# Kernel optimization log

Measured on AMD Instinct MI355X. Metric: run time of the kernel, lower is better.

The kernel has to match this reference:

```python
import jax, jax.numpy as jnp
import numpy as np

EMBED = 768
HEAD = 64

def setup_inputs() -> dict:
    key = jax.random.key(0)
    k1, k2, k3, k4 = jax.random.split(key, 4)
    x = jax.random.normal(k1, (8, 2048, EMBED), dtype=jnp.float32)
    # torch nn.Linear weights: [out, in], applied as x @ W.T
    scale = 1.0 / np.sqrt(EMBED)
    Wq = jax.random.uniform(k2, (HEAD, EMBED), jnp.float32, -scale, scale)
    Wk = jax.random.uniform(k3, (HEAD, EMBED), jnp.float32, -scale, scale)
    Wv = jax.random.uniform(k4, (HEAD, EMBED), jnp.float32, -scale, scale)
    return {"x": x, "Wq": Wq, "Wk": Wk, "Wv": Wv}

def reference(x, Wq, Wk, Wv):
    B, S, E = x.shape
    q = jnp.einsum('bse,he->bsh', x, Wq)
    k = jnp.einsum('bse,he->bsh', x, Wk)
    v = jnp.einsum('bse,he->bsh', x, Wv)
    # NOTE: faithful to source: weights / embed**(-0.5) == weights * sqrt(embed)
    scores = jnp.einsum('bqh,bkh->bqk', q, k) * jnp.sqrt(jnp.float32(E))
    causal = jnp.tril(jnp.ones((S, S), dtype=bool))
    scores = jnp.where(causal, scores, -jnp.inf)
    attn = jax.nn.softmax(scores, axis=-1)
    return jnp.einsum('bqk,bkh->bqh', attn, v)
```

## Files before the change

### kernel.cpp

```cpp
#include <hip/hip_runtime.h>
#include <math.h>

#define EMBED 768
#define SEQ   2048
#define NB    8
#define QSCALE 39.98113776623437f

typedef short  short4v __attribute__((ext_vector_type(4)));
typedef short  short8 __attribute__((ext_vector_type(8)));
typedef float  f32x4  __attribute__((ext_vector_type(4)));
typedef float  f32x16 __attribute__((ext_vector_type(16)));
typedef unsigned int uint2v __attribute__((ext_vector_type(2)));

#define WHI_OFF  0u
#define WLO_OFF  147456u
#define QHI_OFF  294912u
#define QLO_OFF  (294912u + 1u*1048576u)
#define KHI_OFF  (294912u + 2u*1048576u)
#define KLO_OFF  (294912u + 3u*1048576u)
#define VT_OFF   (294912u + 4u*1048576u)
#define OPU_OFF  5537792u
#define MPL_OFF  (5537792u + 8u*1048576u)

__device__ __forceinline__ ushort f2bf(float f) {
    unsigned u = __float_as_uint(f);
    return (ushort)((u + 0x7FFFu + ((u >> 16) & 1u)) >> 16);
}
__device__ __forceinline__ ushort f2bf_trunc(float f) {
    return (ushort)(__float_as_uint(f) >> 16);
}
__device__ __forceinline__ float bf2f(ushort h) {
    return __uint_as_float(((unsigned)h) << 16);
}
__device__ __forceinline__ uint cvtpk(float a, float b) {
    uint r;
    asm("v_cvt_pk_bf16_f32 %0, %1, %2" : "=v"(r) : "v"(a), "v"(b));
    return r;
}

union U8 { uint u[4]; short8 s; };

__global__ __launch_bounds__(256)
void split_w_kernel(const float* __restrict__ Wq, const float* __restrict__ Wk,
                    const float* __restrict__ Wv,
                    ushort* __restrict__ w_hi, ushort* __restrict__ w_lo)
{
    int idx = blockIdx.x * 256 + threadIdx.x;
    if (idx >= 192 * EMBED) return;
    int row = idx / EMBED, e = idx - row * EMBED;
    float f;
    if (row < 64)       f = Wq[row * EMBED + e] * QSCALE;
    else if (row < 128) f = Wk[(row - 64) * EMBED + e];
    else                f = Wv[(row - 128) * EMBED + e];
    ushort hi = f2bf(f);
    w_hi[idx] = hi;
    w_lo[idx] = f2bf_trunc(f - bf2f(hi));
}

__global__ __launch_bounds__(512)
void proj_kernel(const float* __restrict__ x,
                 const ushort* __restrict__ w_hi, const ushort* __restrict__ w_lo,
                 ushort* __restrict__ q_hi, ushort* __restrict__ q_lo,
                 ushort* __restrict__ k_hi, ushort* __restrict__ k_lo,
                 ushort* __restrict__ v_t)
{
    __shared__ __align__(16) ushort xah[2][64][72], xal[2][64][72];
    __shared__ __align__(16) ushort wbh[2][192][72];
    __shared__ __align__(16) ushort wbl[2][128][72];

    const int t    = threadIdx.x;
    const int lane = t & 63;
    const int wid  = t >> 6;
    const int wm   = wid >> 2;
    const int wn   = wid & 3;
    const int ln   = lane & 15;
    const int kg   = lane >> 4;
    const int row0 = blockIdx.x * 64;

#define LOADSET(e0, XR0, XR1, WH0, WH1, WH2, WL0, WL1) do {                       \
        const float* xp_ = x + (size_t)(row0 + (t >> 4)) * EMBED + (e0) + (t & 15) * 4; \
        XR0 = *(const float4*)xp_;                                                \
        XR1 = *(const float4*)(xp_ + 32 * EMBED);                                 \
        const ushort* wp_ = w_hi + (size_t)(t >> 3) * EMBED + (e0) + (t & 7) * 8; \
        WH0 = *(const short8*)wp_;                                                \
        WH1 = *(const short8*)(wp_ + 64 * EMBED);                                 \
        WH2 = *(const short8*)(wp_ + 128 * EMBED);                                \
        const ushort* lp_ = w_lo + (size_t)(t >> 3) * EMBED + (e0) + (t & 7) * 8; \
        WL0 = *(const short8*)lp_;                                                \
        WL1 = *(const short8*)(lp_ + 64 * EMBED);                                 \
    } while (0)

#define STORESET(BUF, XR0, XR1, WH0, WH1, WH2, WL0, WL1) do {                     \
        const int xr_ = t >> 4, xc_ = (t & 15) * 4;                               \
        const float f0_[4] = {XR0.x, XR0.y, XR0.z, XR0.w};                        \
        const float f1_[4] = {XR1.x, XR1.y, XR1.z, XR1.w};                        \
        short4v h0_, l0_, h1_, l1_;                                               \
        _Pragma("unroll")                                                         \
        for (int i_ = 0; i_ < 4; ++i_) {                                          \
            ushort h_ = f2bf(f0_[i_]);                                            \
            h0_[i_] = (short)h_;                                                  \
            l0_[i_] = (short)f2bf_trunc(f0_[i_] - bf2f(h_));                      \
        }                                                                         \
        _Pragma("unroll")                                                         \
        for (int i_ = 0; i_ < 4; ++i_) {                                          \
            ushort h_ = f2bf(f1_[i_]);                                            \
            h1_[i_] = (short)h_;                                                  \
            l1_[i_] = (short)f2bf_trunc(f1_[i_] - bf2f(h_));                      \
        }                                                                         \
        *(short4v*)&xah[BUF][xr_][xc_]      = h0_;                                \
        *(short4v*)&xal[BUF][xr_][xc_]      = l0_;                                \
        *(short4v*)&xah[BUF][xr_ + 32][xc_] = h1_;                                \
        *(short4v*)&xal[BUF][xr_ + 32][xc_] = l1_;                                \
        const int wr_ = t >> 3, wc_ = (t & 7) * 8;                                \
        *(short8*)&wbh[BUF][wr_][wc_]       = WH0;                                \
        *(short8*)&wbh[BUF][wr_ + 64][wc_]  = WH1;                                \
        *(short8*)&wbh[BUF][wr_ + 128][wc_] = WH2;                                \
        *(short8*)&wbl[BUF][wr_][wc_]       = WL0;                                \
        *(short8*)&wbl[BUF][wr_ + 64][wc_]  = WL1;                                \
    } while (0)

#define COMPUTE(BUF) do {                                                         \
        short8 ah_[2][2], al_[2][2];                                              \
        _Pragma("unroll")                                                         \
        for (int mt_ = 0; mt_ < 2; ++mt_)                                         \
            _Pragma("unroll")                                                     \
            for (int ks_ = 0; ks_ < 2; ++ks_) {                                   \
                ah_[mt_][ks_] = *(const short8*)&xah[BUF][wm * 32 + mt_ * 16 + ln][ks_ * 32 + kg * 8]; \
                al_[mt_][ks_] = *(const short8*)&xal[BUF][wm * 32 + mt_ * 16 + ln][ks_ * 32 + kg * 8]; \
            }                                                                     \
        _Pragma("unroll")                                                         \
        for (int j_ = 0; j_ < 3; ++j_) {                                          \
            const int ntg_ = j_ * 4 + wn;                                         \
            _Pragma("unroll")                                                     \
            for (int ks_ = 0; ks_ < 2; ++ks_) {                                   \
                const int co_ = ks_ * 32 + kg * 8;                                \
                short8 bh_ = *(const short8*)&wbh[BUF][ntg_ * 16 + ln][co_];      \
                _Pragma("unroll")                                                 \
                for (int mt_ = 0; mt_ < 2; ++mt_)                                 \
                    acc[mt_][j_] = __builtin_amdgcn_mfma_f32_16x16x32_bf16(ah_[mt_][ks_], bh_, acc[mt_][j_], 0, 0, 0); \
                if (j_ < 2) {                                                     \
                    short8 bl_ = *(const short8*)&wbl[BUF][ntg_ * 16 + ln][co_];  \
                    _Pragma("unroll")                                             \
                    for (int mt_ = 0; mt_ < 2; ++mt_) {                           \
                        acc[mt_][j_] = __builtin_amdgcn_mfma_f32_16x16x32_bf16(ah_[mt_][ks_], bl_, acc[mt_][j_], 0, 0, 0); \
                        acc[mt_][j_] = __builtin_amdgcn_mfma_f32_16x16x32_bf16(al_[mt_][ks_], bh_, acc[mt_][j_], 0, 0, 0); \
                    }                                                             \
                }                                                                 \
            }                                                                     \
        }                                                                         \
    } while (0)

    const f32x4 vzero = {0.f, 0.f, 0.f, 0.f};
    f32x4 acc[2][3];
#pragma unroll
    for (int mt = 0; mt < 2; ++mt)
#pragma unroll
        for (int j = 0; j < 3; ++j) acc[mt][j] = vzero;

    float4 xrA0, xrA1; short8 whA0, whA1, whA2, wlA0, wlA1;
    float4 xrB0, xrB1; short8 whB0, whB1, whB2, wlB0, wlB1;
    float4 xrC0, xrC1; short8 whC0, whC1, whC2, wlC0, wlC1;

    LOADSET(0,   xrA0, xrA1, whA0, whA1, whA2, wlA0, wlA1);
    LOADSET(64,  xrB0, xrB1, whB0, whB1, whB2, wlB0, wlB1);
    LOADSET(128, xrC0, xrC1, whC0, whC1, whC2, wlC0, wlC1);

#define ITER(C_, VMC, BUF, X0, X1, W0, W1, W2, L0, L1) do {                       \
        asm volatile("s_waitcnt vmcnt(" #VMC ")" ::: "memory");                   \
        STORESET(BUF, X0, X1, W0, W1, W2, L0, L1);                                \
        asm volatile("s_waitcnt lgkmcnt(0)" ::: "memory");                        \
        __builtin_amdgcn_s_barrier();                                             \
        if ((C_) + 3 < 12) LOADSET(((C_) + 3) * 64, X0, X1, W0, W1, W2, L0, L1);  \
        COMPUTE(BUF);                                                             \
    } while (0)

    ITER(0,  14, 0, xrA0, xrA1, whA0, whA1, whA2, wlA0, wlA1);
    ITER(1,  14, 1, xrB0, xrB1, whB0, whB1, whB2, wlB0, wlB1);
    ITER(2,  14, 0, xrC0, xrC1, whC0, whC1, whC2, wlC0, wlC1);
    ITER(3,  14, 1, xrA0, xrA1, whA0, whA1, whA2, wlA0, wlA1);
    ITER(4,  14, 0, xrB0, xrB1, whB0, whB1, whB2, wlB0, wlB1);
    ITER(5,  14, 1, xrC0, xrC1, whC0, whC1, whC2, wlC0, wlC1);
    ITER(6,  14, 0, xrA0, xrA1, whA0, whA1, whA2, wlA0, wlA1);
    ITER(7,  14, 1, xrB0, xrB1, whB0, whB1, whB2, wlB0, wlB1);
    ITER(8,  14, 0, xrC0, xrC1, whC0, whC1, whC2, wlC0, wlC1);
    ITER(9,  14, 1, xrA0, xrA1, whA0, whA1, whA2, wlA0, wlA1);
    ITER(10,  7, 0, xrB0, xrB1, whB0, whB1, whB2, wlB0, wlB1);
    ITER(11,  0, 1, xrC0, xrC1, whC0, whC1, whC2, wlC0, wlC1);
#undef ITER
#undef LOADSET
#undef STORESET
#undef COMPUTE

#pragma unroll
    for (int mt = 0; mt < 2; ++mt) {
        const int rbase = row0 + wm * 32 + mt * 16 + kg * 4;
#pragma unroll
        for (int j = 0; j < 3; ++j) {
            const int col = (j * 4 + wn) * 16 + ln;
#pragma unroll
            for (int r = 0; r < 4; ++r) {
                int rg = rbase + r;
                int b = rg >> 11, s = rg & 2047;
                size_t rowoff = ((size_t)b * SEQ + s) * 64;
                float val = acc[mt][j][r];
                if (col < 64) {
                    ushort h = f2bf(val);
                    q_hi[rowoff + col] = h;
                    q_lo[rowoff + col] = f2bf_trunc(val - bf2f(h));
                } else if (col < 128) {
                    ushort h = f2bf(val);
                    k_hi[rowoff + (col - 64)] = h;
                    k_lo[rowoff + (col - 64)] = f2bf_trunc(val - bf2f(h));
                } else {
                    v_t[((size_t)b * 64 + (col - 128)) * SEQ + s] = f2bf(val);
                }
            }
        }
    }
}

__global__ __launch_bounds__(256)
void attn_kernel(const ushort* __restrict__ q_hi, const ushort* __restrict__ q_lo,
                 const ushort* __restrict__ k_hi, const ushort* __restrict__ k_lo,
                 const ushort* __restrict__ v_t,
                 ushort* __restrict__ oP, float* __restrict__ mP,
                 float* __restrict__ lP, int Z)
{
    __shared__ __align__(16) ushort kv[3][3][64][64];

    const int t    = threadIdx.x;
    const int lane = t & 63;
    const int w    = t >> 6;
    const int l31  = lane & 31;
    const int h8   = (lane >> 5) << 3;
    const int sw   = (lane & 7) << 3;
    const int b    = blockIdx.x & 7;
    const int pr   = (blockIdx.x >> 3) & 7;
    const int z    = blockIdx.x >> 6;
    const int qA   = 15 - pr;
    const int qB   = pr;
    const int cA   = 2 * qA + 2;
    const int T    = 34;

    const ushort* qhb = q_hi + (size_t)b * SEQ * 64;
    const ushort* qlb = q_lo + (size_t)b * SEQ * 64;
    const ushort* khb = k_hi + (size_t)b * SEQ * 64;
    const ushort* klb = k_lo + (size_t)b * SEQ * 64;
    const ushort* vtb = v_t + (size_t)b * 64 * SEQ;
    ushort* oPz = oP + (size_t)z * 1048576u;
    float*  mPz = mP + (size_t)z * 16384u;
    float*  lPz = lP + (size_t)z * 16384u;

    const int srow8 = lane >> 3;
    const int scol  = ((lane & 7) << 3) ^ ((lane >> 3) << 3);

    auto stage = [&](int g, int cbuf) {
        const int kk = (g < cA) ? g : g - cA;
        const int j0 = kk << 6;
        ushort* base = &kv[cbuf][0][0][0];
#pragma unroll
        for (int s = 0; s < 6; ++s) {
            const int i = w * 6 + s;
            const int row = ((i & 7) << 3) + srow8;
            const ushort* gp;
            if (i < 8)       gp = khb + (size_t)(j0 + row) * 64 + scol;
            else if (i < 16) gp = klb + (size_t)(j0 + row) * 64 + scol;
            else             gp = vtb + (size_t)row * SEQ + j0 + scol;
            __builtin_amdgcn_global_load_lds(
                (const __attribute__((address_space(1))) void*)gp,
                (__attribute__((address_space(3))) void*)(base + i * 512),
                16, 0, 0);
        }
    };

    auto loadQ = [&](int qb, short8 (&qh)[4], short8 (&ql)[4]) {
#pragma unroll
        for (int ks = 0; ks < 4; ++ks) {
            size_t off = (size_t)(qb * 128 + w * 32 + l31) * 64 + ks * 16 + h8;
            qh[ks] = *(const short8*)(qhb + off);
            ql[ks] = *(const short8*)(qlb + off);
        }
// ... 142 lines not shown
        __builtin_amdgcn_s_barrier();
        if (i + 2 < cnt) stage(z + (i + 2) * Z, (i + 2) % 3);
        if (g >= cA && !inB) {
            storeP(qA, o, m_run, l_run);
            loadQ(qB, qh, ql);
#pragma unroll
            for (int j = 0; j < 16; ++j) { o[0][j] = 0.f; o[1][j] = 0.f; }
            m_run = -INFINITY; l_run = 0.f;
            inB = true;
        }
        body(g < cA ? g : g - cA, g < cA ? qA : qB, o, m_run, l_run, qh, ql, i % 3);
    }

    if (!inB) {
        storeP(qA, o, m_run, l_run);
        const size_t rowq = (size_t)b * SEQ + qB * 128 + w * 32 + l31;
        ushort* op = oPz + rowq * 64;
        const int hb = (lane >> 5) << 2;
#pragma unroll
        for (int ht = 0; ht < 2; ++ht)
#pragma unroll
            for (int rq = 0; rq < 4; ++rq) {
                *(uint*)(op + ht * 32 + rq * 8 + hb)     = 0u;
                *(uint*)(op + ht * 32 + rq * 8 + hb + 2) = 0u;
            }
        if (lane < 32) { mPz[rowq] = -INFINITY; lPz[rowq] = 0.f; }
    } else {
        storeP(qB, o, m_run, l_run);
    }
}

__global__ __launch_bounds__(256)
void merge_kernel(const ushort* __restrict__ oP, const float* __restrict__ mP,
                  const float* __restrict__ lP, float* __restrict__ out, int Z)
{
    int idx = blockIdx.x * 256 + threadIdx.x;
    int R  = idx >> 4;
    int h0 = (idx & 15) << 2;
    float M = -INFINITY;
    for (int zz = 0; zz < Z; ++zz) M = fmaxf(M, mP[zz * 16384 + R]);
    float L = 0.f;
    float4 acc = make_float4(0.f, 0.f, 0.f, 0.f);
    for (int zz = 0; zz < Z; ++zz) {
        float c = exp2f(mP[zz * 16384 + R] - M);
        L += lP[zz * 16384 + R] * c;
        const ushort* op = oP + (size_t)zz * 1048576u + (size_t)R * 64 + h0;
        uint u0 = *(const uint*)op;
        uint u1 = *(const uint*)(op + 2);
        acc.x += bf2f((ushort)(u0 & 0xFFFFu)) * c;
        acc.y += bf2f((ushort)(u0 >> 16))     * c;
        acc.z += bf2f((ushort)(u1 & 0xFFFFu)) * c;
        acc.w += bf2f((ushort)(u1 >> 16))     * c;
    }
    float inv = 1.0f / L;
    float4 r = make_float4(acc.x * inv, acc.y * inv, acc.z * inv, acc.w * inv);
    *(float4*)(out + (size_t)R * 64 + h0) = r;
}

extern "C" void kernel_launch(void* const* d_in, const int* in_sizes, int n_in,
                              void* d_out, int out_size, void* d_ws, size_t ws_size,
                              hipStream_t stream)
{
    const float* x  = (const float*)d_in[0];
    const float* Wq = (const float*)d_in[1];
    const float* Wk = (const float*)d_in[2];
    const float* Wv = (const float*)d_in[3];
    float* out = (float*)d_out;

    ushort* ws = (ushort*)d_ws;
    ushort* w_hi = ws + WHI_OFF;
    ushort* w_lo = ws + WLO_OFF;
    ushort* q_hi = ws + QHI_OFF;
    ushort* q_lo = ws + QLO_OFF;
    ushort* k_hi = ws + KHI_OFF;
    ushort* k_lo = ws + KLO_OFF;
    ushort* v_t  = ws + VT_OFF;

    const int Z = 8;
    ushort* oP = ws + OPU_OFF;
    float*  mP = (float*)(ws + MPL_OFF);
    float*  lP = mP + (size_t)Z * 16384u;

    split_w_kernel<<<dim3(576), dim3(256), 0, stream>>>(Wq, Wk, Wv, w_hi, w_lo);
    proj_kernel<<<dim3(256), dim3(512), 0, stream>>>(x, w_hi, w_lo,
                                                     q_hi, q_lo, k_hi, k_lo, v_t);
    attn_kernel<<<dim3(64 * Z), dim3(256), 0, stream>>>(q_hi, q_lo, k_hi, k_lo, v_t,
                                                        oP, mP, lP, Z);
    merge_kernel<<<dim3(1024), dim3(256), 0, stream>>>(oP, mP, lP, out, Z);
}
```

Baseline: 55.58 us.

## Load weights via direct global-to-LDS with swizzle; split x in registers

The projection kernel now copies the bf16 hi/lo weight tiles straight into LDS with global_load_lds into a triple-buffered, XOR-swizzled layout. x is no longer staged through shared memory: each lane loads its own MFMA fragment rows from global and splits them into bf16 hi/lo pairs in registers with packed converts. The pipeline changes to a two-stage prefetch, and MFMA sections run at raised priority. This removes the LDS stores and the lgkmcnt wait for x and the weights. In exchange, the per-lane x loads are less coalesced and use more registers.

After: 69.03 us. 24.2% more time.

```diff
diff --git a/kernel.cpp b/kernel.cpp
--- a/kernel.cpp
+++ b/kernel.cpp
@@ -6,7 +6,6 @@
 #define NB    8
 #define QSCALE 39.98113776623437f
 
-typedef short  short4v __attribute__((ext_vector_type(4)));
 typedef short  short8 __attribute__((ext_vector_type(8)));
 typedef float  f32x4  __attribute__((ext_vector_type(4)));
 typedef float  f32x16 __attribute__((ext_vector_type(16)));
@@ -36,6 +35,12 @@
     uint r;
     asm("v_cvt_pk_bf16_f32 %0, %1, %2" : "=v"(r) : "v"(a), "v"(b));
     return r;
+}
+__device__ __forceinline__ float pklo(uint h) {
+    return __uint_as_float(h << 16);
+}
+__device__ __forceinline__ float pkhi(uint h) {
+    return __uint_as_float(h & 0xFFFF0000u);
 }
 
 union U8 { uint u[4]; short8 s; };
@@ -64,9 +69,7 @@
                  ushort* __restrict__ k_hi, ushort* __restrict__ k_lo,
                  ushort* __restrict__ v_t)
 {
-    __shared__ __align__(16) ushort xah[2][64][72], xal[2][64][72];
-    __shared__ __align__(16) ushort wbh[2][192][72];
-    __shared__ __align__(16) ushort wbl[2][128][72];
+    __shared__ __align__(16) ushort wb[3][20480];
 
     const int t    = threadIdx.x;
     const int lane = t & 63;
@@ -77,118 +80,126 @@
     const int kg   = lane >> 4;
     const int row0 = blockIdx.x * 64;
 
-#define LOADSET(e0, XR0, XR1, WH0, WH1, WH2, WL0, WL1) do {                       \
-        const float* xp_ = x + (size_t)(row0 + (t >> 4)) * EMBED + (e0) + (t & 15) * 4; \
-        XR0 = *(const float4*)xp_;                                                \
-        XR1 = *(const float4*)(xp_ + 32 * EMBED);                                 \
-        const ushort* wp_ = w_hi + (size_t)(t >> 3) * EMBED + (e0) + (t & 7) * 8; \
-        WH0 = *(const short8*)wp_;                                                \
-        WH1 = *(const short8*)(wp_ + 64 * EMBED);                                 \
-        WH2 = *(const short8*)(wp_ + 128 * EMBED);                                \
-        const ushort* lp_ = w_lo + (size_t)(t >> 3) * EMBED + (e0) + (t & 7) * 8; \
-        WL0 = *(const short8*)lp_;                                                \
-        WL1 = *(const short8*)(lp_ + 64 * EMBED);                                 \
+    const int srow8 = lane >> 3;
+    const int scol  = ((lane & 7) << 3) ^ ((lane >> 3) << 3);
+
+    auto stageW = [&](int c, int bf) {
+        const int e0 = c * 64;
+        ushort* base = &wb[bf][0];
+#pragma unroll
+        for (int s = 0; s < 5; ++s) {
+            const int i = wid * 5 + s;
+            if (i < 24) {
+                const int row = i * 8 + srow8;
+                const ushort* gp = w_hi + (size_t)row * EMBED + e0 + scol;
+                __builtin_amdgcn_global_load_lds(
+                    (const __attribute__((address_space(1))) void*)gp,
+                    (__attribute__((address_space(3))) void*)(base + i * 512),
+                    16, 0, 0);
+            } else {
+                const int il = i - 24;
+                const int row = il * 8 + srow8;
+                const ushort* gp = w_lo + (size_t)row * EMBED + e0 + scol;
+                __builtin_amdgcn_global_load_lds(
+                    (const __attribute__((address_space(1))) void*)gp,
+                    (__attribute__((address_space(3))) void*)(base + 12288 + il * 512),
+                    16, 0, 0);
+            }
+        }
+    };
+
+#define XLOAD(e0, R) do {                                                        \
+        const float* xp_ = x + (size_t)(row0 + wm * 32 + ln) * EMBED + (e0) + kg * 8; \
+        R[0] = *(const float4*)xp_;                                              \
+        R[1] = *(const float4*)(xp_ + 4);                                        \
+        R[2] = *(const float4*)(xp_ + 32);                                       \
+        R[3] = *(const float4*)(xp_ + 36);                                       \
+        R[4] = *(const float4*)(xp_ + 16 * EMBED);                               \
+        R[5] = *(const float4*)(xp_ + 16 * EMBED + 4);                           \
+        R[6] = *(const float4*)(xp_ + 16 * EMBED + 32);                          \
+        R[7] = *(const float4*)(xp_ + 16 * EMBED + 36);                          \
     } while (0)
 
-#define STORESET(BUF, XR0, XR1, WH0, WH1, WH2, WL0, WL1) do {                     \
-        const int xr_ = t >> 4, xc_ = (t & 15) * 4;                               \
-        const float f0_[4] = {XR0.x, XR0.y, XR0.z, XR0.w};                        \
-        const float f1_[4] = {XR1.x, XR1.y, XR1.z, XR1.w};                        \
-        short4v h0_, l0_, h1_, l1_;                                               \
-        _Pragma("unroll")                                                         \
-        for (int i_ = 0; i_ < 4; ++i_) {                                          \
-            ushort h_ = f2bf(f0_[i_]);                                            \
-            h0_[i_] = (short)h_;                                                  \
-            l0_[i_] = (short)f2bf_trunc(f0_[i_] - bf2f(h_));                      \
-        }                                                                         \
-        _Pragma("unroll")                                                         \
-        for (int i_ = 0; i_ < 4; ++i_) {                                          \
-            ushort h_ = f2bf(f1_[i_]);                                            \
-            h1_[i_] = (short)h_;                                                  \
-            l1_[i_] = (short)f2bf_trunc(f1_[i_] - bf2f(h_));                      \
-        }                                                                         \
-        *(short4v*)&xah[BUF][xr_][xc_]      = h0_;                                \
-        *(short4v*)&xal[BUF][xr_][xc_]      = l0_;                                \
-        *(short4v*)&xah[BUF][xr_ + 32][xc_] = h1_;                                \
-        *(short4v*)&xal[BUF][xr_ + 32][xc_] = l1_;                                \
-        const int wr_ = t >> 3, wc_ = (t & 7) * 8;                                \
-        *(short8*)&wbh[BUF][wr_][wc_]       = WH0;                                \
-        *(short8*)&wbh[BUF][wr_ + 64][wc_]  = WH1;                                \
-        *(short8*)&wbh[BUF][wr_ + 128][wc_] = WH2;                                \
-        *(short8*)&wbl[BUF][wr_][wc_]       = WL0;                                \
-        *(short8*)&wbl[BUF][wr_ + 64][wc_]  = WL1;                                \
-    } while (0)
-
-#define COMPUTE(BUF) do {                                                         \
-        short8 ah_[2][2], al_[2][2];                                              \
+    const f32x4 vzero = {0.f, 0.f, 0.f, 0.f};
+    f32x4 acc[2][3];
+#pragma unroll
+    for (int mt = 0; mt < 2; ++mt)
+#pragma unroll
+        for (int j = 0; j < 3; ++j) acc[mt][j] = vzero;
+
+#define COMPUTE(BF, R) do {                                                       \
+        const ushort* WHB_ = &wb[BF][0];                                          \
+        const ushort* WLB_ = &wb[BF][12288];                                      \
+        U8 ah_[2][2], al_[2][2];                                                  \
         _Pragma("unroll")                                                         \
         for (int mt_ = 0; mt_ < 2; ++mt_)                                         \
             _Pragma("unroll")                                                     \
             for (int ks_ = 0; ks_ < 2; ++ks_) {                                   \
-                ah_[mt_][ks_] = *(const short8*)&xah[BUF][wm * 32 + mt_ * 16 + ln][ks_ * 32 + kg * 8]; \
-                al_[mt_][ks_] = *(const short8*)&xal[BUF][wm * 32 + mt_ * 16 + ln][ks_ * 32 + kg * 8]; \
+                float4 a_ = R[mt_ * 4 + ks_ * 2];                                 \
+                float4 b_ = R[mt_ * 4 + ks_ * 2 + 1];                             \
+                U8 H_, L_;                                                        \
+                H_.u[0] = cvtpk(a_.x, a_.y);  H_.u[1] = cvtpk(a_.z, a_.w);        \
+                H_.u[2] = cvtpk(b_.x, b_.y);  H_.u[3] = cvtpk(b_.z, b_.w);        \
+                L_.u[0] = cvtpk(a_.x - pklo(H_.u[0]), a_.y - pkhi(H_.u[0]));      \
+                L_.u[1] = cvtpk(a_.z - pklo(H_.u[1]), a_.w - pkhi(H_.u[1]));      \
+                L_.u[2] = cvtpk(b_.x - pklo(H_.u[2]), b_.y - pkhi(H_.u[2]));      \
+                L_.u[3] = cvtpk(b_.z - pklo(H_.u[3]), b_.w - pkhi(H_.u[3]));      \
+                ah_[mt_][ks_] = H_;  al_[mt_][ks_] = L_;                          \
             }                                                                     \
+        __builtin_amdgcn_s_setprio(1);                                            \
         _Pragma("unroll")                                                         \
         for (int j_ = 0; j_ < 3; ++j_) {                                          \
             const int ntg_ = j_ * 4 + wn;                                         \
             _Pragma("unroll")                                                     \
             for (int ks_ = 0; ks_ < 2; ++ks_) {                                   \
-                const int co_ = ks_ * 32 + kg * 8;                                \
-                short8 bh_ = *(const short8*)&wbh[BUF][ntg_ * 16 + ln][co_];      \
+                const int rw_  = ntg_ * 16 + ln;                                  \
+                const int off_ = rw_ * 64 + ((ks_ * 32 + kg * 8) ^ ((rw_ & 7) << 3)); \
+                short8 bh_ = *(const short8*)(WHB_ + off_);                       \
                 _Pragma("unroll")                                                 \
                 for (int mt_ = 0; mt_ < 2; ++mt_)                                 \
-                    acc[mt_][j_] = __builtin_amdgcn_mfma_f32_16x16x32_bf16(ah_[mt_][ks_], bh_, acc[mt_][j_], 0, 0, 0); \
+                    acc[mt_][j_] = __builtin_amdgcn_mfma_f32_16x16x32_bf16(ah_[mt_][ks_].s, bh_, acc[mt_][j_], 0, 0, 0); \
                 if (j_ < 2) {                                                     \
-                    short8 bl_ = *(const short8*)&wbl[BUF][ntg_ * 16 + ln][co_];  \
+                    short8 bl_ = *(const short8*)(WLB_ + off_);                   \
                     _Pragma("unroll")                                             \
                     for (int mt_ = 0; mt_ < 2; ++mt_) {                           \
-                        acc[mt_][j_] = __builtin_amdgcn_mfma_f32_16x16x32_bf16(ah_[mt_][ks_], bl_, acc[mt_][j_], 0, 0, 0); \
-                        acc[mt_][j_] = __builtin_amdgcn_mfma_f32_16x16x32_bf16(al_[mt_][ks_], bh_, acc[mt_][j_], 0, 0, 0); \
+                        acc[mt_][j_] = __builtin_amdgcn_mfma_f32_16x16x32_bf16(ah_[mt_][ks_].s, bl_, acc[mt_][j_], 0, 0, 0); \
+                        acc[mt_][j_] = __builtin_amdgcn_mfma_f32_16x16x32_bf16(al_[mt_][ks_].s, bh_, acc[mt_][j_], 0, 0, 0); \
                     }                                                             \
                 }                                                                 \
             }                                                                     \
         }                                                                         \
+        __builtin_amdgcn_s_setprio(0);                                            \
     } while (0)
 
-    const f32x4 vzero = {0.f, 0.f, 0.f, 0.f};
-    f32x4 acc[2][3];
-#pragma unroll
-    for (int mt = 0; mt < 2; ++mt)
-#pragma unroll
-        for (int j = 0; j < 3; ++j) acc[mt][j] = vzero;
-
-    float4 xrA0, xrA1; short8 whA0, whA1, whA2, wlA0, wlA1;
-    float4 xrB0, xrB1; short8 whB0, whB1, whB2, wlB0, wlB1;
-    float4 xrC0, xrC1; short8 whC0, whC1, whC2, wlC0, wlC1;
-
-    LOADSET(0,   xrA0, xrA1, whA0, whA1, whA2, wlA0, wlA1);
-    LOADSET(64,  xrB0, xrB1, whB0, whB1, whB2, wlB0, wlB1);
-    LOADSET(128, xrC0, xrC1, whC0, whC1, whC2, wlC0, wlC1);
-
-#define ITER(C_, VMC, BUF, X0, X1, W0, W1, W2, L0, L1) do {                       \
+    float4 xr0[8], xr1[8], xr2[8];
+
+    stageW(0, 0); XLOAD(0,  xr0);
+    stageW(1, 1); XLOAD(64, xr1);
+
+#define ITER(C_, VMC, RSET, RNEXT) do {                                           \
         asm volatile("s_waitcnt vmcnt(" #VMC ")" ::: "memory");                   \
-        STORESET(BUF, X0, X1, W0, W1, W2, L0, L1);                                \
-        asm volatile("s_waitcnt lgkmcnt(0)" ::: "memory");                        \
         __builtin_amdgcn_s_barrier();                                             \
-        if ((C_) + 3 < 12) LOADSET(((C_) + 3) * 64, X0, X1, W0, W1, W2, L0, L1);  \
-        COMPUTE(BUF);                                                             \
+        if ((C_) + 2 < 12) {                                                      \
+            stageW((C_) + 2, ((C_) + 2) % 3);                                     \
+            XLOAD(((C_) + 2) * 64, RNEXT);                                        \
+        }                                                                         \
+        COMPUTE((C_) % 3, RSET);                                                  \
     } while (0)
 
-    ITER(0,  14, 0, xrA0, xrA1, whA0, whA1, whA2, wlA0, wlA1);
-    ITER(1,  14, 1, xrB0, xrB1, whB0, whB1, whB2, wlB0, wlB1);
-    ITER(2,  14, 0, xrC0, xrC1, whC0, whC1, whC2, wlC0, wlC1);
-    ITER(3,  14, 1, xrA0, xrA1, whA0, whA1, whA2, wlA0, wlA1);
-    ITER(4,  14, 0, xrB0, xrB1, whB0, whB1, whB2, wlB0, wlB1);
-    ITER(5,  14, 1, xrC0, xrC1, whC0, whC1, whC2, wlC0, wlC1);
-    ITER(6,  14, 0, xrA0, xrA1, whA0, whA1, whA2, wlA0, wlA1);
-    ITER(7,  14, 1, xrB0, xrB1, whB0, whB1, whB2, wlB0, wlB1);
-    ITER(8,  14, 0, xrC0, xrC1, whC0, whC1, whC2, wlC0, wlC1);
-    ITER(9,  14, 1, xrA0, xrA1, whA0, whA1, whA2, wlA0, wlA1);
-    ITER(10,  7, 0, xrB0, xrB1, whB0, whB1, whB2, wlB0, wlB1);
-    ITER(11,  0, 1, xrC0, xrC1, whC0, whC1, whC2, wlC0, wlC1);
+    ITER(0,  13, xr0, xr2);
+    ITER(1,  13, xr1, xr0);
+    ITER(2,  13, xr2, xr1);
+    ITER(3,  13, xr0, xr2);
+    ITER(4,  13, xr1, xr0);
+    ITER(5,  13, xr2, xr1);
+    ITER(6,  13, xr0, xr2);
+    ITER(7,  13, xr1, xr0);
+    ITER(8,  13, xr2, xr1);
+    ITER(9,  13, xr0, xr2);
+    ITER(10, 13, xr1, xr0);
+    ITER(11,  0, xr2, xr0);
 #undef ITER
-#undef LOADSET
-#undef STORESET
+#undef XLOAD
 #undef COMPUTE
 
 #pragma unroll
```

## Shrink projection tiles to 32 rows and 32-wide K steps for more blocks

Applied to the files above, without the earlier changes.

The projection kernel now uses 256-thread blocks covering 32 rows each, with 32-wide K chunks over 24 pipelined iterations, so the grid grows from 256 to 512 blocks to better fill the GPU's compute units. It also raises wave priority around the MFMA section with s_setprio. The cost is that each block re-reads the full weight matrix for half as many rows, doubling weight traffic, and each K step does less work per barrier, so barrier overhead grows.

Result: slower. 66.80 us (+20.2%).

```diff
diff --git a/kernel.cpp b/kernel.cpp
--- a/kernel.cpp
+++ b/kernel.cpp
@@ -57,61 +57,49 @@
     w_lo[idx] = f2bf_trunc(f - bf2f(hi));
 }
 
-__global__ __launch_bounds__(512)
+__global__ __launch_bounds__(256)
 void proj_kernel(const float* __restrict__ x,
                  const ushort* __restrict__ w_hi, const ushort* __restrict__ w_lo,
                  ushort* __restrict__ q_hi, ushort* __restrict__ q_lo,
                  ushort* __restrict__ k_hi, ushort* __restrict__ k_lo,
                  ushort* __restrict__ v_t)
 {
-    __shared__ __align__(16) ushort xah[2][64][72], xal[2][64][72];
-    __shared__ __align__(16) ushort wbh[2][192][72];
-    __shared__ __align__(16) ushort wbl[2][128][72];
+    __shared__ __align__(16) ushort xah[2][32][40], xal[2][32][40];
+    __shared__ __align__(16) ushort wbh[2][192][40];
+    __shared__ __align__(16) ushort wbl[2][128][40];
 
     const int t    = threadIdx.x;
     const int lane = t & 63;
-    const int wid  = t >> 6;
-    const int wm   = wid >> 2;
-    const int wn   = wid & 3;
+    const int w    = t >> 6;
     const int ln   = lane & 15;
     const int kg   = lane >> 4;
-    const int row0 = blockIdx.x * 64;
-
-#define LOADSET(e0, XR0, XR1, WH0, WH1, WH2, WL0, WL1) do {                       \
-        const float* xp_ = x + (size_t)(row0 + (t >> 4)) * EMBED + (e0) + (t & 15) * 4; \
-        XR0 = *(const float4*)xp_;                                                \
-        XR1 = *(const float4*)(xp_ + 32 * EMBED);                                 \
-        const ushort* wp_ = w_hi + (size_t)(t >> 3) * EMBED + (e0) + (t & 7) * 8; \
+    const int row0 = blockIdx.x * 32;
+
+#define LOADSET(e0, XR, WH0, WH1, WH2, WL0, WL1) do {                             \
+        const float* xp_ = x + (size_t)(row0 + (t >> 3)) * EMBED + (e0) + (t & 7) * 4; \
+        XR = *(const float4*)xp_;                                                 \
+        const ushort* wp_ = w_hi + (size_t)(t >> 2) * EMBED + (e0) + (t & 3) * 8; \
         WH0 = *(const short8*)wp_;                                                \
         WH1 = *(const short8*)(wp_ + 64 * EMBED);                                 \
         WH2 = *(const short8*)(wp_ + 128 * EMBED);                                \
-        const ushort* lp_ = w_lo + (size_t)(t >> 3) * EMBED + (e0) + (t & 7) * 8; \
+        const ushort* lp_ = w_lo + (size_t)(t >> 2) * EMBED + (e0) + (t & 3) * 8; \
         WL0 = *(const short8*)lp_;                                                \
         WL1 = *(const short8*)(lp_ + 64 * EMBED);                                 \
     } while (0)
 
-#define STORESET(BUF, XR0, XR1, WH0, WH1, WH2, WL0, WL1) do {                     \
-        const int xr_ = t >> 4, xc_ = (t & 15) * 4;                               \
-        const float f0_[4] = {XR0.x, XR0.y, XR0.z, XR0.w};                        \
-        const float f1_[4] = {XR1.x, XR1.y, XR1.z, XR1.w};                        \
-        short4v h0_, l0_, h1_, l1_;                                               \
+#define STORESET(BUF, XR, WH0, WH1, WH2, WL0, WL1) do {                           \
+        const int xr_ = t >> 3, xc_ = (t & 7) * 4;                                \
+        const float fv_[4] = {XR.x, XR.y, XR.z, XR.w};                            \
+        short4v h_, l_;                                                           \
         _Pragma("unroll")                                                         \
         for (int i_ = 0; i_ < 4; ++i_) {                                          \
-            ushort h_ = f2bf(f0_[i_]);                                            \
-            h0_[i_] = (short)h_;                                                  \
-            l0_[i_] = (short)f2bf_trunc(f0_[i_] - bf2f(h_));                      \
+            ushort hh_ = f2bf(fv_[i_]);                                           \
+            h_[i_] = (short)hh_;                                                  \
+            l_[i_] = (short)f2bf_trunc(fv_[i_] - bf2f(hh_));                      \
         }                                                                         \
-        _Pragma("unroll")                                                         \
-        for (int i_ = 0; i_ < 4; ++i_) {                                          \
-            ushort h_ = f2bf(f1_[i_]);                                            \
-            h1_[i_] = (short)h_;                                                  \
-            l1_[i_] = (short)f2bf_trunc(f1_[i_] - bf2f(h_));                      \
-        }                                                                         \
-        *(short4v*)&xah[BUF][xr_][xc_]      = h0_;                                \
-        *(short4v*)&xal[BUF][xr_][xc_]      = l0_;                                \
-        *(short4v*)&xah[BUF][xr_ + 32][xc_] = h1_;                                \
-        *(short4v*)&xal[BUF][xr_ + 32][xc_] = l1_;                                \
-        const int wr_ = t >> 3, wc_ = (t & 7) * 8;                                \
+        *(short4v*)&xah[BUF][xr_][xc_] = h_;                                      \
+        *(short4v*)&xal[BUF][xr_][xc_] = l_;                                      \
+        const int wr_ = t >> 2, wc_ = (t & 3) * 8;                                \
         *(short8*)&wbh[BUF][wr_][wc_]       = WH0;                                \
         *(short8*)&wbh[BUF][wr_ + 64][wc_]  = WH1;                                \
         *(short8*)&wbh[BUF][wr_ + 128][wc_] = WH2;                                \
@@ -120,34 +108,30 @@
     } while (0)
 
 #define COMPUTE(BUF) do {                                                         \
-        short8 ah_[2][2], al_[2][2];                                              \
+        short8 ah_[2], al_[2];                                                    \
         _Pragma("unroll")                                                         \
-        for (int mt_ = 0; mt_ < 2; ++mt_)                                         \
-            _Pragma("unroll")                                                     \
-            for (int ks_ = 0; ks_ < 2; ++ks_) {                                   \
-                ah_[mt_][ks_] = *(const short8*)&xah[BUF][wm * 32 + mt_ * 16 + ln][ks_ * 32 + kg * 8]; \
-                al_[mt_][ks_] = *(const short8*)&xal[BUF][wm * 32 + mt_ * 16 + ln][ks_ * 32 + kg * 8]; \
-            }                                                                     \
+        for (int mt_ = 0; mt_ < 2; ++mt_) {                                       \
+            ah_[mt_] = *(const short8*)&xah[BUF][mt_ * 16 + ln][kg * 8];          \
+            al_[mt_] = *(const short8*)&xal[BUF][mt_ * 16 + ln][kg * 8];          \
+        }                                                                         \
+        __builtin_amdgcn_s_setprio(1);                                            \
         _Pragma("unroll")                                                         \
         for (int j_ = 0; j_ < 3; ++j_) {                                          \
-            const int ntg_ = j_ * 4 + wn;                                         \
+            const int ntg_ = j_ * 4 + w;                                          \
+            short8 bh_ = *(const short8*)&wbh[BUF][ntg_ * 16 + ln][kg * 8];       \
             _Pragma("unroll")                                                     \
-            for (int ks_ = 0; ks_ < 2; ++ks_) {                                   \
-                const int co_ = ks_ * 32 + kg * 8;                                \
-                short8 bh_ = *(const short8*)&wbh[BUF][ntg_ * 16 + ln][co_];      \
+            for (int mt_ = 0; mt_ < 2; ++mt_)                                     \
+                acc[mt_][j_] = __builtin_amdgcn_mfma_f32_16x16x32_bf16(ah_[mt_], bh_, acc[mt_][j_], 0, 0, 0); \
+            if (j_ < 2) {                                                         \
+                short8 bl_ = *(const short8*)&wbl[BUF][ntg_ * 16 + ln][kg * 8];   \
                 _Pragma("unroll")                                                 \
-                for (int mt_ = 0; mt_ < 2; ++mt_)                                 \
-                    acc[mt_][j_] = __builtin_amdgcn_mfma_f32_16x16x32_bf16(ah_[mt_][ks_], bh_, acc[mt_][j_], 0, 0, 0); \
-                if (j_ < 2) {                                                     \
-                    short8 bl_ = *(const short8*)&wbl[BUF][ntg_ * 16 + ln][co_];  \
-                    _Pragma("unroll")                                             \
-                    for (int mt_ = 0; mt_ < 2; ++mt_) {                           \
-                        acc[mt_][j_] = __builtin_amdgcn_mfma_f32_16x16x32_bf16(ah_[mt_][ks_], bl_, acc[mt_][j_], 0, 0, 0); \
-                        acc[mt_][j_] = __builtin_amdgcn_mfma_f32_16x16x32_bf16(al_[mt_][ks_], bh_, acc[mt_][j_], 0, 0, 0); \
-                    }                                                             \
+                for (int mt_ = 0; mt_ < 2; ++mt_) {                               \
+                    acc[mt_][j_] = __builtin_amdgcn_mfma_f32_16x16x32_bf16(ah_[mt_], bl_, acc[mt_][j_], 0, 0, 0); \
+                    acc[mt_][j_] = __builtin_amdgcn_mfma_f32_16x16x32_bf16(al_[mt_], bh_, acc[mt_][j_], 0, 0, 0); \
                 }                                                                 \
             }                                                                     \
         }                                                                         \
+        __builtin_amdgcn_s_setprio(0);                                            \
     } while (0)
 
     const f32x4 vzero = {0.f, 0.f, 0.f, 0.f};
@@ -157,35 +141,47 @@
 #pragma unroll
         for (int j = 0; j < 3; ++j) acc[mt][j] = vzero;
 
-    float4 xrA0, xrA1; short8 whA0, whA1, whA2, wlA0, wlA1;
-    float4 xrB0, xrB1; short8 whB0, whB1, whB2, wlB0, wlB1;
-    float4 xrC0, xrC1; short8 whC0, whC1, whC2, wlC0, wlC1;
-
-    LOADSET(0,   xrA0, xrA1, whA0, whA1, whA2, wlA0, wlA1);
-    LOADSET(64,  xrB0, xrB1, whB0, whB1, whB2, wlB0, wlB1);
-    LOADSET(128, xrC0, xrC1, whC0, whC1, whC2, wlC0, wlC1);
-
-#define ITER(C_, VMC, BUF, X0, X1, W0, W1, W2, L0, L1) do {                       \
+    float4 xA; short8 hA0, hA1, hA2, lA0, lA1;
+    float4 xB; short8 hB0, hB1, hB2, lB0, lB1;
+    float4 xC; short8 hC0, hC1, hC2, lC0, lC1;
+
+    LOADSET(0,  xA, hA0, hA1, hA2, lA0, lA1);
+    LOADSET(32, xB, hB0, hB1, hB2, lB0, lB1);
+    LOADSET(64, xC, hC0, hC1, hC2, lC0, lC1);
+
+#define ITER(C_, VMC, XR, W0, W1, W2, L0, L1) do {                                \
         asm volatile("s_waitcnt vmcnt(" #VMC ")" ::: "memory");                   \
-        STORESET(BUF, X0, X1, W0, W1, W2, L0, L1);                                \
+        STORESET((C_) & 1, XR, W0, W1, W2, L0, L1);                               \
         asm volatile("s_waitcnt lgkmcnt(0)" ::: "memory");                        \
         __builtin_amdgcn_s_barrier();                                             \
-        if ((C_) + 3 < 12) LOADSET(((C_) + 3) * 64, X0, X1, W0, W1, W2, L0, L1);  \
-        COMPUTE(BUF);                                                             \
+        if ((C_) + 3 < 24) LOADSET(((C_) + 3) * 32, XR, W0, W1, W2, L0, L1);      \
+        COMPUTE((C_) & 1);                                                        \
     } while (0)
 
-    ITER(0,  14, 0, xrA0, xrA1, whA0, whA1, whA2, wlA0, wlA1);
-    ITER(1,  14, 1, xrB0, xrB1, whB0, whB1, whB2, wlB0, wlB1);
-    ITER(2,  14, 0, xrC0, xrC1, whC0, whC1, whC2, wlC0, wlC1);
-    ITER(3,  14, 1, xrA0, xrA1, whA0, whA1, whA2, wlA0, wlA1);
-    ITER(4,  14, 0, xrB0, xrB1, whB0, whB1, whB2, wlB0, wlB1);
-    ITER(5,  14, 1, xrC0, xrC1, whC0, whC1, whC2, wlC0, wlC1);
-    ITER(6,  14, 0, xrA0, xrA1, whA0, whA1, whA2, wlA0, wlA1);
-    ITER(7,  14, 1, xrB0, xrB1, whB0, whB1, whB2, wlB0, wlB1);
-    ITER(8,  14, 0, xrC0, xrC1, whC0, whC1, whC2, wlC0, wlC1);
-    ITER(9,  14, 1, xrA0, xrA1, whA0, whA1, whA2, wlA0, wlA1);
-    ITER(10,  7, 0, xrB0, xrB1, whB0, whB1, whB2, wlB0, wlB1);
-    ITER(11,  0, 1, xrC0, xrC1, whC0, whC1, whC2, wlC0, wlC1);
+    ITER(0,  12, xA, hA0, hA1, hA2, lA0, lA1);
+    ITER(1,  12, xB, hB0, hB1, hB2, lB0, lB1);
+    ITER(2,  12, xC, hC0, hC1, hC2, lC0, lC1);
+    ITER(3,  12, xA, hA0, hA1, hA2, lA0, lA1);
+    ITER(4,  12, xB, hB0, hB1, hB2, lB0, lB1);
+    ITER(5,  12, xC, hC0, hC1, hC2, lC0, lC1);
+    ITER(6,  12, xA, hA0, hA1, hA2, lA0, lA1);
+    ITER(7,  12, xB, hB0, hB1, hB2, lB0, lB1);
+    ITER(8,  12, xC, hC0, hC1, hC2, lC0, lC1);
+    ITER(9,  12, xA, hA0, hA1, hA2, lA0, lA1);
+    ITER(10, 12, xB, hB0, hB1, hB2, lB0, lB1);
+    ITER(11, 12, xC, hC0, hC1, hC2, lC0, lC1);
+    ITER(12, 12, xA, hA0, hA1, hA2, lA0, lA1);
+    ITER(13, 12, xB, hB0, hB1, hB2, lB0, lB1);
+    ITER(14, 12, xC, hC0, hC1, hC2, lC0, lC1);
+    ITER(15, 12, xA, hA0, hA1, hA2, lA0, lA1);
+    ITER(16, 12, xB, hB0, hB1, hB2, lB0, lB1);
+    ITER(17, 12, xC, hC0, hC1, hC2, lC0, lC1);
+    ITER(18, 12, xA, hA0, hA1, hA2, lA0, lA1);
+    ITER(19, 12, xB, hB0, hB1, hB2, lB0, lB1);
+    ITER(20, 12, xC, hC0, hC1, hC2, lC0, lC1);
+    ITER(21, 12, xA, hA0, hA1, hA2, lA0, lA1);
+    ITER(22,  6, xB, hB0, hB1, hB2, lB0, lB1);
+    ITER(23,  0, xC, hC0, hC1, hC2, lC0, lC1);
 #undef ITER
 #undef LOADSET
 #undef STORESET
@@ -193,10 +189,10 @@
 
 #pragma unroll
     for (int mt = 0; mt < 2; ++mt) {
-        const int rbase = row0 + wm * 32 + mt * 16 + kg * 4;
+        const int rbase = row0 + mt * 16 + kg * 4;
 #pragma unroll
         for (int j = 0; j < 3; ++j) {
-            const int col = (j * 4 + wn) * 16 + ln;
+            const int col = (j * 4 + w) * 16 + ln;
 #pragma unroll
             for (int r = 0; r < 4; ++r) {
                 int rg = rbase + r;
@@ -505,7 +501,7 @@
     float*  lP = mP + (size_t)Z * 16384u;
 
     split_w_kernel<<<dim3(576), dim3(256), 0, stream>>>(Wq, Wk, Wv, w_hi, w_lo);
-    proj_kernel<<<dim3(256), dim3(512), 0, stream>>>(x, w_hi, w_lo,
+    proj_kernel<<<dim3(512), dim3(256), 0, stream>>>(x, w_hi, w_lo,
                                                      q_hi, q_lo, k_hi, k_lo, v_t);
     attn_kernel<<<dim3(64 * Z), dim3(256), 0, stream>>>(q_hi, q_lo, k_hi, k_lo, v_t,
                                                         oP, mP, lP, Z);
```

## Shrink projection tile to 32 rows and load W_lo fragments straight to registers

Applied to the files above, without the earlier changes.

The projection kernel now uses 32-row tiles with 256 threads over 512 blocks instead of 64-row tiles with 512 threads over 256 blocks. The low-part weight fragments for Q and K are loaded from global memory directly into MFMA operand registers, so the wbl shared buffer goes away. The prefetch of the next chunk is moved to after the compute, and the compute phase is wrapped in raised wave priority (s_setprio). The intent is to cut LDS traffic and footprint and to spread the work over more blocks, at the cost of more register pressure and of reading W_hi again for every 32-row tile.

Measured after the change: 61.54 us. +10.7%, slower.

```diff
diff --git a/kernel.cpp b/kernel.cpp
--- a/kernel.cpp
+++ b/kernel.cpp
@@ -57,89 +57,85 @@
     w_lo[idx] = f2bf_trunc(f - bf2f(hi));
 }
 
-__global__ __launch_bounds__(512)
+__global__ __launch_bounds__(256)
 void proj_kernel(const float* __restrict__ x,
                  const ushort* __restrict__ w_hi, const ushort* __restrict__ w_lo,
                  ushort* __restrict__ q_hi, ushort* __restrict__ q_lo,
                  ushort* __restrict__ k_hi, ushort* __restrict__ k_lo,
                  ushort* __restrict__ v_t)
 {
-    __shared__ __align__(16) ushort xah[2][64][72], xal[2][64][72];
+    __shared__ __align__(16) ushort xah[2][32][72], xal[2][32][72];
     __shared__ __align__(16) ushort wbh[2][192][72];
-    __shared__ __align__(16) ushort wbl[2][128][72];
 
     const int t    = threadIdx.x;
     const int lane = t & 63;
-    const int wid  = t >> 6;
-    const int wm   = wid >> 2;
-    const int wn   = wid & 3;
+    const int w    = t >> 6;
     const int ln   = lane & 15;
     const int kg   = lane >> 4;
-    const int row0 = blockIdx.x * 64;
-
-#define LOADSET(e0, XR0, XR1, WH0, WH1, WH2, WL0, WL1) do {                       \
-        const float* xp_ = x + (size_t)(row0 + (t >> 4)) * EMBED + (e0) + (t & 15) * 4; \
+    const int row0 = blockIdx.x * 32;
+
+#define LOADSET(e0, XR0, XR1, WH0, WH1, WH2, WH3, WH4, WH5, WQ0, WQ1, WK0, WK1) do { \
+        const float* xp_ = x + (size_t)(row0 + (t >> 3)) * EMBED + (e0) + (t & 7) * 8; \
         XR0 = *(const float4*)xp_;                                                \
-        XR1 = *(const float4*)(xp_ + 32 * EMBED);                                 \
-        const ushort* wp_ = w_hi + (size_t)(t >> 3) * EMBED + (e0) + (t & 7) * 8; \
+        XR1 = *(const float4*)(xp_ + 4);                                          \
+        const ushort* wp_ = w_hi + (size_t)(t >> 2) * EMBED + (e0) + (t & 3) * 16; \
         WH0 = *(const short8*)wp_;                                                \
-        WH1 = *(const short8*)(wp_ + 64 * EMBED);                                 \
-        WH2 = *(const short8*)(wp_ + 128 * EMBED);                                \
-        const ushort* lp_ = w_lo + (size_t)(t >> 3) * EMBED + (e0) + (t & 7) * 8; \
-        WL0 = *(const short8*)lp_;                                                \
-        WL1 = *(const short8*)(lp_ + 64 * EMBED);                                 \
+        WH1 = *(const short8*)(wp_ + 8);                                          \
+        WH2 = *(const short8*)(wp_ + 64 * EMBED);                                 \
+        WH3 = *(const short8*)(wp_ + 64 * EMBED + 8);                             \
+        WH4 = *(const short8*)(wp_ + 128 * EMBED);                                \
+        WH5 = *(const short8*)(wp_ + 128 * EMBED + 8);                            \
+        const ushort* lq_ = w_lo + (size_t)(w * 16 + ln) * EMBED + (e0) + kg * 8;       \
+        WQ0 = *(const short8*)lq_;                                                \
+        WQ1 = *(const short8*)(lq_ + 32);                                         \
+        const ushort* lk_ = w_lo + (size_t)((4 + w) * 16 + ln) * EMBED + (e0) + kg * 8; \
+        WK0 = *(const short8*)lk_;                                                \
+        WK1 = *(const short8*)(lk_ + 32);                                         \
     } while (0)
 
-#define STORESET(BUF, XR0, XR1, WH0, WH1, WH2, WL0, WL1) do {                     \
-        const int xr_ = t >> 4, xc_ = (t & 15) * 4;                               \
-        const float f0_[4] = {XR0.x, XR0.y, XR0.z, XR0.w};                        \
-        const float f1_[4] = {XR1.x, XR1.y, XR1.z, XR1.w};                        \
-        short4v h0_, l0_, h1_, l1_;                                               \
+#define STORESET(BUF, XR0, XR1, WH0, WH1, WH2, WH3, WH4, WH5) do {                \
+        const int xr_ = t >> 3, xc_ = (t & 7) * 8;                                \
+        const float fv_[8] = {XR0.x, XR0.y, XR0.z, XR0.w,                         \
+                              XR1.x, XR1.y, XR1.z, XR1.w};                        \
+        short8 h_, l_;                                                            \
         _Pragma("unroll")                                                         \
-        for (int i_ = 0; i_ < 4; ++i_) {                                          \
-            ushort h_ = f2bf(f0_[i_]);                                            \
-            h0_[i_] = (short)h_;                                                  \
-            l0_[i_] = (short)f2bf_trunc(f0_[i_] - bf2f(h_));                      \
+        for (int i_ = 0; i_ < 8; ++i_) {                                          \
+            ushort hh_ = f2bf(fv_[i_]);                                           \
+            h_[i_] = (short)hh_;                                                  \
+            l_[i_] = (short)f2bf_trunc(fv_[i_] - bf2f(hh_));                      \
         }                                                                         \
-        _Pragma("unroll")                                                         \
-        for (int i_ = 0; i_ < 4; ++i_) {                                          \
-            ushort h_ = f2bf(f1_[i_]);                                            \
-            h1_[i_] = (short)h_;                                                  \
-            l1_[i_] = (short)f2bf_trunc(f1_[i_] - bf2f(h_));                      \
-        }                                                                         \
-        *(short4v*)&xah[BUF][xr_][xc_]      = h0_;                                \
-        *(short4v*)&xal[BUF][xr_][xc_]      = l0_;                                \
-        *(short4v*)&xah[BUF][xr_ + 32][xc_] = h1_;                                \
-        *(short4v*)&xal[BUF][xr_ + 32][xc_] = l1_;                                \
-        const int wr_ = t >> 3, wc_ = (t & 7) * 8;                                \
-        *(short8*)&wbh[BUF][wr_][wc_]       = WH0;                                \
-        *(short8*)&wbh[BUF][wr_ + 64][wc_]  = WH1;                                \
-        *(short8*)&wbh[BUF][wr_ + 128][wc_] = WH2;                                \
-        *(short8*)&wbl[BUF][wr_][wc_]       = WL0;                                \
-        *(short8*)&wbl[BUF][wr_ + 64][wc_]  = WL1;                                \
+        *(short8*)&xah[BUF][xr_][xc_] = h_;                                       \
+        *(short8*)&xal[BUF][xr_][xc_] = l_;                                       \
+        const int wr_ = t >> 2, wc_ = (t & 3) * 16;                               \
+        *(short8*)&wbh[BUF][wr_][wc_]           = WH0;                            \
+        *(short8*)&wbh[BUF][wr_][wc_ + 8]       = WH1;                            \
+        *(short8*)&wbh[BUF][wr_ + 64][wc_]      = WH2;                            \
+        *(short8*)&wbh[BUF][wr_ + 64][wc_ + 8]  = WH3;                            \
+        *(short8*)&wbh[BUF][wr_ + 128][wc_]     = WH4;                            \
+        *(short8*)&wbh[BUF][wr_ + 128][wc_ + 8] = WH5;                            \
     } while (0)
 
-#define COMPUTE(BUF) do {                                                         \
+#define COMPUTE(BUF, WQ0, WQ1, WK0, WK1) do {                                     \
         short8 ah_[2][2], al_[2][2];                                              \
         _Pragma("unroll")                                                         \
         for (int mt_ = 0; mt_ < 2; ++mt_)                                         \
             _Pragma("unroll")                                                     \
             for (int ks_ = 0; ks_ < 2; ++ks_) {                                   \
-                ah_[mt_][ks_] = *(const short8*)&xah[BUF][wm * 32 + mt_ * 16 + ln][ks_ * 32 + kg * 8]; \
-                al_[mt_][ks_] = *(const short8*)&xal[BUF][wm * 32 + mt_ * 16 + ln][ks_ * 32 + kg * 8]; \
+                ah_[mt_][ks_] = *(const short8*)&xah[BUF][mt_ * 16 + ln][ks_ * 32 + kg * 8]; \
+                al_[mt_][ks_] = *(const short8*)&xal[BUF][mt_ * 16 + ln][ks_ * 32 + kg * 8]; \
             }                                                                     \
+        __builtin_amdgcn_s_setprio(1);                                            \
         _Pragma("unroll")                                                         \
         for (int j_ = 0; j_ < 3; ++j_) {                                          \
-            const int ntg_ = j_ * 4 + wn;                                         \
+            const int ntg_ = j_ * 4 + w;                                          \
             _Pragma("unroll")                                                     \
             for (int ks_ = 0; ks_ < 2; ++ks_) {                                   \
-                const int co_ = ks_ * 32 + kg * 8;                                \
-                short8 bh_ = *(const short8*)&wbh[BUF][ntg_ * 16 + ln][co_];      \
+                short8 bh_ = *(const short8*)&wbh[BUF][ntg_ * 16 + ln][ks_ * 32 + kg * 8]; \
                 _Pragma("unroll")                                                 \
                 for (int mt_ = 0; mt_ < 2; ++mt_)                                 \
                     acc[mt_][j_] = __builtin_amdgcn_mfma_f32_16x16x32_bf16(ah_[mt_][ks_], bh_, acc[mt_][j_], 0, 0, 0); \
                 if (j_ < 2) {                                                     \
-                    short8 bl_ = *(const short8*)&wbl[BUF][ntg_ * 16 + ln][co_];  \
+                    short8 bl_ = (j_ == 0) ? (ks_ ? WQ1 : WQ0) : (ks_ ? WK1 : WK0); \
                     _Pragma("unroll")                                             \
                     for (int mt_ = 0; mt_ < 2; ++mt_) {                           \
                         acc[mt_][j_] = __builtin_amdgcn_mfma_f32_16x16x32_bf16(ah_[mt_][ks_], bl_, acc[mt_][j_], 0, 0, 0); \
@@ -148,6 +144,7 @@
                 }                                                                 \
             }                                                                     \
         }                                                                         \
+        __builtin_amdgcn_s_setprio(0);                                            \
     } while (0)
 
     const f32x4 vzero = {0.f, 0.f, 0.f, 0.f};
@@ -157,35 +154,35 @@
 #pragma unroll
         for (int j = 0; j < 3; ++j) acc[mt][j] = vzero;
 
-    float4 xrA0, xrA1; short8 whA0, whA1, whA2, wlA0, wlA1;
-    float4 xrB0, xrB1; short8 whB0, whB1, whB2, wlB0, wlB1;
-    float4 xrC0, xrC1; short8 whC0, whC1, whC2, wlC0, wlC1;
-
-    LOADSET(0,   xrA0, xrA1, whA0, whA1, whA2, wlA0, wlA1);
-    LOADSET(64,  xrB0, xrB1, whB0, whB1, whB2, wlB0, wlB1);
-    LOADSET(128, xrC0, xrC1, whC0, whC1, whC2, wlC0, wlC1);
-
-#define ITER(C_, VMC, BUF, X0, X1, W0, W1, W2, L0, L1) do {                       \
+    float4 xA0, xA1; short8 hA0, hA1, hA2, hA3, hA4, hA5, qA0, qA1, kA0, kA1;
+    float4 xB0, xB1; short8 hB0, hB1, hB2, hB3, hB4, hB5, qB0, qB1, kB0, kB1;
+    float4 xC0, xC1; short8 hC0, hC1, hC2, hC3, hC4, hC5, qC0, qC1, kC0, kC1;
+
+    LOADSET(0,   xA0, xA1, hA0, hA1, hA2, hA3, hA4, hA5, qA0, qA1, kA0, kA1);
+    LOADSET(64,  xB0, xB1, hB0, hB1, hB2, hB3, hB4, hB5, qB0, qB1, kB0, kB1);
+    LOADSET(128, xC0, xC1, hC0, hC1, hC2, hC3, hC4, hC5, qC0, qC1, kC0, kC1);
+
+#define ITER(C_, VMC, X0, X1, W0, W1, W2, W3, W4, W5, Q0, Q1, K0, K1) do {        \
         asm volatile("s_waitcnt vmcnt(" #VMC ")" ::: "memory");                   \
-        STORESET(BUF, X0, X1, W0, W1, W2, L0, L1);                                \
+        STORESET((C_) & 1, X0, X1, W0, W1, W2, W3, W4, W5);                       \
         asm volatile("s_waitcnt lgkmcnt(0)" ::: "memory");                        \
         __builtin_amdgcn_s_barrier();                                             \
-        if ((C_) + 3 < 12) LOADSET(((C_) + 3) * 64, X0, X1, W0, W1, W2, L0, L1);  \
-        COMPUTE(BUF);                                                             \
+        COMPUTE((C_) & 1, Q0, Q1, K0, K1);                                        \
+        if ((C_) + 3 < 12) LOADSET(((C_) + 3) * 64, X0, X1, W0, W1, W2, W3, W4, W5, Q0, Q1, K0, K1); \
     } while (0)
 
-    ITER(0,  14, 0, xrA0, xrA1, whA0, whA1, whA2, wlA0, wlA1);
-    ITER(1,  14, 1, xrB0, xrB1, whB0, whB1, whB2, wlB0, wlB1);
-    ITER(2,  14, 0, xrC0, xrC1, whC0, whC1, whC2, wlC0, wlC1);
-    ITER(3,  14, 1, xrA0, xrA1, whA0, whA1, whA2, wlA0, wlA1);
-    ITER(4,  14, 0, xrB0, xrB1, whB0, whB1, whB2, wlB0, wlB1);
-    ITER(5,  14, 1, xrC0, xrC1, whC0, whC1, whC2, wlC0, wlC1);
-    ITER(6,  14, 0, xrA0, xrA1, whA0, whA1, whA2, wlA0, wlA1);
-    ITER(7,  14, 1, xrB0, xrB1, whB0, whB1, whB2, wlB0, wlB1);
-    ITER(8,  14, 0, xrC0, xrC1, whC0, whC1, whC2, wlC0, wlC1);
-    ITER(9,  14, 1, xrA0, xrA1, whA0, whA1, whA2, wlA0, wlA1);
-    ITER(10,  7, 0, xrB0, xrB1, whB0, whB1, whB2, wlB0, wlB1);
-    ITER(11,  0, 1, xrC0, xrC1, whC0, whC1, whC2, wlC0, wlC1);
+    ITER(0,  24, xA0, xA1, hA0, hA1, hA2, hA3, hA4, hA5, qA0, qA1, kA0, kA1);
+    ITER(1,  24, xB0, xB1, hB0, hB1, hB2, hB3, hB4, hB5, qB0, qB1, kB0, kB1);
+    ITER(2,  24, xC0, xC1, hC0, hC1, hC2, hC3, hC4, hC5, qC0, qC1, kC0, kC1);
+    ITER(3,  24, xA0, xA1, hA0, hA1, hA2, hA3, hA4, hA5, qA0, qA1, kA0, kA1);
+    ITER(4,  24, xB0, xB1, hB0, hB1, hB2, hB3, hB4, hB5, qB0, qB1, kB0, kB1);
+    ITER(5,  24, xC0, xC1, hC0, hC1, hC2, hC3, hC4, hC5, qC0, qC1, kC0, kC1);
+    ITER(6,  24, xA0, xA1, hA0, hA1, hA2, hA3, hA4, hA5, qA0, qA1, kA0, kA1);
+    ITER(7,  24, xB0, xB1, hB0, hB1, hB2, hB3, hB4, hB5, qB0, qB1, kB0, kB1);
+    ITER(8,  24, xC0, xC1, hC0, hC1, hC2, hC3, hC4, hC5, qC0, qC1, kC0, kC1);
+    ITER(9,  24, xA0, xA1, hA0, hA1, hA2, hA3, hA4, hA5, qA0, qA1, kA0, kA1);
+    ITER(10, 12, xB0, xB1, hB0, hB1, hB2, hB3, hB4, hB5, qB0, qB1, kB0, kB1);
+    ITER(11,  0, xC0, xC1, hC0, hC1, hC2, hC3, hC4, hC5, qC0, qC1, kC0, kC1);
 #undef ITER
 #undef LOADSET
 #undef STORESET
@@ -193,10 +190,10 @@
 
 #pragma unroll
     for (int mt = 0; mt < 2; ++mt) {
-        const int rbase = row0 + wm * 32 + mt * 16 + kg * 4;
+        const int rbase = row0 + mt * 16 + kg * 4;
 #pragma unroll
         for (int j = 0; j < 3; ++j) {
-            const int col = (j * 4 + wn) * 16 + ln;
+            const int col = (j * 4 + w) * 16 + ln;
 #pragma unroll
             for (int r = 0; r < 4; ++r) {
                 int rg = rbase + r;
@@ -505,7 +502,7 @@
     float*  lP = mP + (size_t)Z * 16384u;
 
     split_w_kernel<<<dim3(576), dim3(256), 0, stream>>>(Wq, Wk, Wv, w_hi, w_lo);
-    proj_kernel<<<dim3(256), dim3(512), 0, stream>>>(x, w_hi, w_lo,
+    proj_kernel<<<dim3(512), dim3(256), 0, stream>>>(x, w_hi, w_lo,
                                                      q_hi, q_lo, k_hi, k_lo, v_t);
     attn_kernel<<<dim3(64 * Z), dim3(256), 0, stream>>>(q_hi, q_lo, k_hi, k_lo, v_t,
                                                         oP, mP, lP, Z);
```
